# Performance work log

Hardware: AMD Instinct MI355X
Metric: run time of the kernel (lower is better)

Reference implementation:

```python
import jax, jax.numpy as jnp
import numpy as np

L = 12      # n_layers
C = 768     # n_embd = dim = dim_att
H = 12      # heads
N = 64      # head_size_a
FF = 2688   # dim_ffn = int(768*3.5//32*32)
P = 2       # patch_size
INCH = 4
IMG = 32
NCLS = 1000
FREQ = 256
HC = C // 2  # conv stem channels (dim//2)
B = 32
D_MIX = 32
D_DEC = 64
LNX_EPS = 1e-5 * 8.0 ** 2  # GroupNorm eps with head_size_divisor=8


def _ln(x, w=None, b=None, eps=1e-5):
    m = x.mean(-1, keepdims=True)
    v = x.var(-1, keepdims=True)
    xh = (x - m) * jax.lax.rsqrt(v + eps)
    if w is not None:
        xh = xh * w + b
    return xh


def _shift(x):  # RWKV token shift: prepend zero row, drop last
    return jnp.pad(x, ((0, 0), (1, 0), (0, 0)))[:, :-1]


def _gn_img(x, w, b, groups=32, eps=1e-5):
    Bb, Ch, Hh, Ww = x.shape
    xg = x.reshape(Bb, groups, Ch // groups, Hh, Ww)
    m = xg.mean((2, 3, 4), keepdims=True)
    v = xg.var((2, 3, 4), keepdims=True)
    xg = (xg - m) * jax.lax.rsqrt(v + eps)
    return xg.reshape(Bb, Ch, Hh, Ww) * w[None, :, None, None] + b[None, :, None, None]


def _conv5(x, w, b):
    y = jax.lax.conv_general_dilated(x, w, (1, 1), ((2, 2), (2, 2)),
                                     dimension_numbers=('NCHW', 'OIHW', 'NCHW'))
    return y + b[None, :, None, None]


def _wkv(r, k, v, w, u):
    # r,k,v,w: (B,T,H,N); u: (H,N). S[b,h,i,j]: key i -> value j.
    def step(S, inp):
        rt, kt, vt, wt = inp  # each (B,H,N)
        kv = kt[..., :, None] * vt[..., None, :]           # (B,H,N,N)
        y = jnp.einsum('bhi,bhij->bhj', rt, S + u[None, :, :, None] * kv)
        S = wt[..., :, None] * S + kv
        return S, y
    S0 = jnp.zeros((r.shape[0], H, N, N), r.dtype)
    seq = tuple(jnp.moveaxis(a, 1, 0) for a in (r, k, v, w))
    _, ys = jax.lax.scan(step, S0, seq)
    return jnp.moveaxis(ys, 0, 1)  # (B,T,H,N)


def _timemix(x, p):
    Bb, Tt, _ = x.shape
    xx = _shift(x) - x
    xxx = x + xx * p['maa'][0]
    mix = jnp.tanh(xxx @ p['tm_w1']).reshape(Bb, Tt, 5, D_MIX)
    m = jnp.einsum('btfd,fdc->fbtc', mix, p['tm_w2'])  # (5,B,T,C): mw,mk,mv,mr,mg
    xw = x + xx * (p['maa'][1] + m[0])
    xk = x + xx * (p['maa'][2] + m[1])
    xv = x + xx * (p['maa'][3] + m[2])
    xr = x + xx * (p['maa'][4] + m[3])
    xg = x + xx * (p['maa'][5] + m[4])
    r = (xr @ p['r_w'].T).reshape(Bb, Tt, H, N)
    k = (xk @ p['k_w'].T).reshape(Bb, Tt, H, N)
    v = (xv @ p['v_w'].T).reshape(Bb, Tt, H, N)
    g = jax.nn.silu(xg @ p['g_w'].T)
    ww = p['td'] + jnp.tanh(xw @ p['td_w1']) @ p['td_w2']
    w = jnp.exp(-jnp.exp(ww)).reshape(Bb, Tt, H, N)
    y = _wkv(r, k, v, w, p['faaaa'])  # (B,T,H,N)
    mn = y.mean(-1, keepdims=True)
    vr = y.var(-1, keepdims=True)
    y = ((y - mn) * jax.lax.rsqrt(vr + LNX_EPS)).reshape(Bb, Tt, C) * p['lnx_w'] + p['lnx_b']
    return (y * g) @ p['o_w'].T


def _chanmix(x, p):
    xx = _shift(x) - x
    xk = x + xx * p['fmaa'][0]
    xr = x + xx * p['fmaa'][1]
    k = jnp.square(jax.nn.relu(xk @ p['fk_w'].T))
    return jax.nn.sigmoid(xr @ p['fr_w'].T) * (k @ p['fv_w'].T)


def _forward(x, t, y, c1_w, c1_b, gn1_w, gn1_b, c2_w, c2_b, gn2_w, gn2_b,
             xe_w, xe_b, te_w1, te_b1, te_w2, te_b2, y_tab, ln0_w, ln0_b,
             ln1_w, ln1_b, ln2_w, ln2_b, att_maa, tm_w1, tm_w2, td, td_w1,
             td_w2, faaaa, r_w, k_w, v_w, o_w, g_w, lnx_w, lnx_b, ffn_maa,
             fk_w, fr_w, fv_w, ada_w, ada_b, fl_ada_w, fl_ada_b, fl_w, fl_b):
    Bb = x.shape[0]
    h = jax.nn.silu(_conv5(x, c1_w, c1_b))
    h = _gn_img(h, gn1_w, gn1_b)
    h = jax.nn.silu(_conv5(h, c2_w, c2_b))
    h = _gn_img(h, gn2_w, gn2_b)
    # patchify: (B,HC,IMG,IMG) -> (B,T,P*P*HC)
    G = IMG // P
    h = h.reshape(Bb, HC, G, P, G, P).transpose(0, 2, 4, 1, 3, 5).reshape(Bb, G * G, HC * P * P)
    xs = h @ xe_w.T + xe_b
    # timestep embedding
    half = FREQ // 2
    freqs = jnp.exp(-jnp.log(10000.0) * jnp.arange(half, dtype=jnp.float32) / half)
    ang = t[:, None] * freqs[None]
    temb = jnp.concatenate([jnp.cos(ang), jnp.sin(ang)], -1)
    temb = jax.nn.silu(temb @ te_w1.T + te_b1) @ te_w2.T + te_b2
    c = temb + y_tab[y]  # adaln_input (B,C)
    for l in range(L):
        ada = jax.nn.silu(c) @ ada_w[l].T + ada_b[l]
        sm, scm, gm, sp, scp, gp = jnp.split(ada, 6, axis=1)
        if l == 0:
            xs = _ln(xs, ln0_w, ln0_b)
        p = dict(maa=att_maa[l], tm_w1=tm_w1[l], tm_w2=tm_w2[l], td=td[l],
                 td_w1=td_w1[l], td_w2=td_w2[l], faaaa=faaaa[l], r_w=r_w[l],
                 k_w=k_w[l], v_w=v_w[l], o_w=o_w[l], g_w=g_w[l], lnx_w=lnx_w[l],
                 lnx_b=lnx_b[l], fmaa=ffn_maa[l], fk_w=fk_w[l], fr_w=fr_w[l],
                 fv_w=fv_w[l])
        hmod = _ln(xs, ln1_w[l], ln1_b[l]) * (1 + scm[:, None, :]) + sm[:, None, :]
        xs = xs + gm[:, None, :] * _timemix(hmod, p)
        hmod = _ln(xs, ln2_w[l], ln2_b[l]) * (1 + scp[:, None, :]) + sp[:, None, :]
        xs = xs + gp[:, None, :] * _chanmix(hmod, p)
    ada = jax.nn.silu(c) @ fl_ada_w.T + fl_ada_b
    sh, sc = jnp.split(ada, 2, axis=1)
    out = (_ln(xs, eps=1e-6) * (1 + sc[:, None, :]) + sh[:, None, :]) @ fl_w.T + fl_b
    G = IMG // P
    out = out.reshape(Bb, G, G, P, P, INCH)
    out = jnp.einsum('nhwpqc->nchpwq', out).reshape(Bb, INCH, IMG, IMG)
    return out


def setup_inputs() -> dict:
    key = jax.random.key(0)
    ks = iter(jax.random.split(key, 64))
    def rn(shape, s=0.02):
        return (jax.random.normal(next(ks), shape) * s).astype(jnp.float32)
    inp = {}
    inp['x'] = jax.random.normal(next(ks), (B, INCH, IMG, IMG), jnp.float32)
    inp['t'] = jax.random.uniform(next(ks), (B,), jnp.float32) * 1000.0
    inp['y'] = jax.random.randint(next(ks), (B,), 0, NCLS)
    inp['c1_w'] = rn((HC, INCH, 5, 5), 0.05); inp['c1_b'] = jnp.zeros(HC)
    inp['gn1_w'] = jnp.ones(HC); inp['gn1_b'] = jnp.zeros(HC)
    inp['c2_w'] = rn((HC, HC, 5, 5), 0.02); inp['c2_b'] = jnp.zeros(HC)
    inp['gn2_w'] = jnp.ones(HC); inp['gn2_b'] = jnp.zeros(HC)
    inp['xe_w'] = rn((C, P * P * HC)); inp['xe_b'] = jnp.zeros(C)
    inp['te_w1'] = rn((C, FREQ)); inp['te_b1'] = jnp.zeros(C)
    inp['te_w2'] = rn((C, C)); inp['te_b2'] = jnp.zeros(C)
    inp['y_tab'] = rn((NCLS + 1, C))
    inp['ln0_w'] = jnp.ones(C); inp['ln0_b'] = jnp.zeros(C)
    inp['ln1_w'] = jnp.ones((L, C)); inp['ln1_b'] = jnp.zeros((L, C))
    inp['ln2_w'] = jnp.ones((L, C)); inp['ln2_b'] = jnp.zeros((L, C))
    inp['att_maa'] = jax.random.uniform(next(ks), (L, 6, C), jnp.float32)
    inp['tm_w1'] = rn((L, C, 5 * D_MIX), 0.01)
    inp['tm_w2'] = rn((L, 5, D_MIX, C), 0.01)
    inp['td'] = rn((L, C), 0.5) - 3.0
    inp['td_w1'] = rn((L, C, D_DEC), 0.01)
    inp['td_w2'] = rn((L, D_DEC, C), 0.01)
    inp['faaaa'] = rn((L, H, N), 0.1)
    for nm in ('r_w', 'k_w', 'v_w', 'o_w', 'g_w'):
        inp[nm] = rn((L, C, C))
    inp['lnx_w'] = jnp.ones((L, C)); inp['lnx_b'] = jnp.zeros((L, C))
    inp['ffn_maa'] = jax.random.uniform(next(ks), (L, 2, C), jnp.float32)
    inp['fk_w'] = rn((L, FF, C)); inp['fr_w'] = rn((L, C, C)); inp['fv_w'] = rn((L, C, FF))
    inp['ada_w'] = rn((L, 6 * C, C)); inp['ada_b'] = jnp.zeros((L, 6 * C))
    inp['fl_ada_w'] = rn((2 * C, C)); inp['fl_ada_b'] = jnp.zeros(2 * C)
    inp['fl_w'] = rn((P * P * INCH, C)); inp['fl_b'] = jnp.zeros(P * P * INCH)
    return inp


def reference(x, t, y, c1_w, c1_b, gn1_w, gn1_b, c2_w, c2_b, gn2_w, gn2_b,
              xe_w, xe_b, te_w1, te_b1, te_w2, te_b2, y_tab, ln0_w, ln0_b,
              ln1_w, ln1_b, ln2_w, ln2_b, att_maa, tm_w1, tm_w2, td, td_w1,
              td_w2, faaaa, r_w, k_w, v_w, o_w, g_w, lnx_w, lnx_b, ffn_maa,
              fk_w, fr_w, fv_w, ada_w, ada_b, fl_ada_w, fl_ada_b, fl_w, fl_b):
    return _forward(x, t, y, c1_w, c1_b, gn1_w, gn1_b, c2_w, c2_b, gn2_w, gn2_b,
                    xe_w, xe_b, te_w1, te_b1, te_w2, te_b2, y_tab, ln0_w, ln0_b,
                    ln1_w, ln1_b, ln2_w, ln2_b, att_maa, tm_w1, tm_w2, td, td_w1,
                    td_w2, faaaa, r_w, k_w, v_w, o_w, g_w, lnx_w, lnx_b, ffn_maa,
                    fk_w, fr_w, fv_w, ada_w, ada_b, fl_ada_w, fl_ada_b, fl_w, fl_b)
```

## Files before the change

kernel.cpp:

```cpp
#include <hip/hip_runtime.h>
#include <math.h>


typedef short  s16x8 __attribute__((ext_vector_type(8)));
typedef float  f32x4 __attribute__((ext_vector_type(4)));
typedef __attribute__((address_space(1))) const void as1_cv;
typedef __attribute__((address_space(3))) void as3_v;

#define GLDS16(gp, lp) __builtin_amdgcn_global_load_lds( \
    (as1_cv*)(unsigned long long)(const void*)(gp), \
    (as3_v*)(unsigned int)(unsigned long long)(void*)(lp), 16, 0, 0)

static __device__ __forceinline__ float sigf(float x){ return 1.f/(1.f+expf(-x)); }
static __device__ __forceinline__ unsigned short f2b(float x){
  unsigned int u = __builtin_bit_cast(unsigned int, x);
  unsigned int r = (u + 0x7FFFu + ((u >> 16) & 1u)) >> 16;
  return (unsigned short)r;
}
static __device__ __forceinline__ float b2f(unsigned short h){
  unsigned int u = ((unsigned int)h)<<16; return __builtin_bit_cast(float,u);
}

static const size_t O_XS    = 0ull;
static const size_t O_HMOD  = 6291456ull;
// ... 199 lines not shown
  const int wr = w >> 1, wc = w & 1;
  const int l15 = lane & 15, l4 = lane >> 4;
  const int kkc = ((lane & 7) ^ (lane >> 3)) * 8;
  const int N = gr.N;
  f32x4 acc[4][4] = {};
  for (int k0 = 0; k0 < K; k0 += 64) {
    #pragma unroll
    for (int i = 0; i < 4; i++) {
      const int rb = i*32 + w*8;
      const int r  = rb + (lane >> 3);
      GLDS16(gr.A + (size_t)(row0 + r)*K + k0 + kkc, &As[rb][0]);
      GLDS16(gr.B + (size_t)(col0 + r)*K + k0 + kkc, &Bs[rb][0]);
    }
    __syncthreads();
    #pragma unroll
    for (int ks = 0; ks < 2; ks++) {
      s16x8 af[4], bf[4];
      #pragma unroll
      for (int m = 0; m < 4; m++) {
        const int r = wr*64 + m*16 + l15;
        const int sl = (ks*4 + l4) ^ (r & 7);
        af[m] = *reinterpret_cast<const s16x8*>(&As[r][sl*8]);
      }
      #pragma unroll
      for (int n = 0; n < 4; n++) {
        const int r = wc*64 + n*16 + l15;
        const int sl = (ks*4 + l4) ^ (r & 7);
        bf[n] = *reinterpret_cast<const s16x8*>(&Bs[r][sl*8]);
      }
      #pragma unroll
      for (int m = 0; m < 4; m++)
        #pragma unroll
        for (int n = 0; n < 4; n++)
          acc[m][n] = __builtin_amdgcn_mfma_f32_16x16x32_bf16(af[m], bf[n], acc[m][n], 0, 0, 0);
    }
    __syncthreads();
  }
  float* Cf = (float*)gr.C; unsigned short* Ch = (unsigned short*)gr.C;
  #pragma unroll
  for (int m = 0; m < 4; m++) {
    const int rbase = row0 + wr*64 + m*16 + (l4<<2);
    #pragma unroll
    for (int n = 0; n < 4; n++) {
      const int c = col0 + wc*64 + n*16 + l15;
      #pragma unroll
      for (int q = 0; q < 4; q++) {
        const int r = rbase + q;
        float v = acc[m][n][q];
        const size_t idx = (size_t)r*N + c;
        switch (gr.epi) {
          case 0: Cf[idx] = v; break;
          case 1: Cf[idx] = v*sigf(v); break;
          case 2: Cf[idx] = sigf(v); break;
          default: { float t=fmaxf(v,0.f); Ch[idx] = f2b(t*t); } break;
        }
      }
    }
  }
}

__global__ __launch_bounds__(256) void conv1_k(
    const float* __restrict__ x, const float* __restrict__ w,
    const float* __restrict__ bias, float* __restrict__ out)
{
  const int blk = blockIdx.x; const int bb = blk / 384; const int oc = blk % 384;
  __shared__ __align__(16) float sIn[4*1296];
  __shared__ __align__(16) float sW[100];
  const int tid = threadIdx.x;
  for (int idx=tid; idx<4*1296; idx+=256){
    int ic = idx/1296; int rem = idx - ic*1296;
    int yy = rem/36, xx = rem - yy*36;
    int gy = yy-2, gx = xx-2;
    float v = 0.f;
    if ((unsigned)gy < 32u && (unsigned)gx < 32u)
      v = x[(((size_t)bb*4+ic)*32+gy)*32+gx];
    sIn[idx]=v;
  }
  if (tid < 100) sW[tid] = w[(size_t)oc*100 + tid];
  __syncthreads();
  const float bv = bias[oc];
  #pragma unroll
  for (int i=0;i<4;i++){
    int p = tid + 256*i; int py=p>>5, px=p&31;
    int pb = py*36+px;
    float acc = bv;
    #pragma unroll
    for (int ic=0;ic<4;ic++)
      #pragma unroll
      for (int ky=0;ky<5;ky++)
        #pragma unroll
        for (int kx=0;kx<5;kx++)
          acc = fmaf(sIn[ic*1296 + pb + ky*36+kx], sW[ic*25+ky*5+kx], acc);
    out[((size_t)(bb*384+oc))*1024 + p] = acc*sigf(acc);
  }
}

__global__ __launch_bounds__(256) void gn_stats_nchw_k(
    const float* __restrict__ h, float* __restrict__ stats)
{
  const int blk = blockIdx.x;
  const size_t base = (size_t)blk*12288;
  const int tid = threadIdx.x;
  float s=0.f, s2=0.f;
  for (int idx=tid; idx<12288; idx+=256){ float v=h[base+idx]; s+=v; s2=fmaf(v,v,s2); }
  #pragma unroll
  for (int mask=32; mask>=1; mask>>=1){ s += __shfl_xor(s,mask); s2 += __shfl_xor(s2,mask); }
  __shared__ float ps[8];
// ... 1 lines not shown
  __syncthreads();
  if (tid==0){
    s = ps[0]+ps[1]+ps[2]+ps[3]; s2 = ps[4]+ps[5]+ps[6]+ps[7];
    float mean = s*(1.f/12288.f);
    float var  = s2*(1.f/12288.f) - mean*mean;
    stats[blk*2] = mean; stats[blk*2+1] = rsqrtf(var + 1e-5f);
  }
}

__global__ void zero16_k(unsigned short* __restrict__ p)
{
  size_t i = ((size_t)blockIdx.x*256 + threadIdx.x)*8;
  *reinterpret_cast<uint4*>(p + i) = make_uint4(0u,0u,0u,0u);
}

__global__ __launch_bounds__(256) void pad_apply_k(
    const float* __restrict__ img1, const float* __restrict__ stats,
    const float* __restrict__ w, const float* __restrict__ bgn,
    unsigned short* __restrict__ pad)
{
  __shared__ float t[8][33];
  const int b = blockIdx.x >> 5, y = blockIdx.x & 31;
  const int tid = threadIdx.x;
  for (int ic0 = 0; ic0 < 384; ic0 += 8) {
    const int icr = tid >> 5, xr = tid & 31;
    t[icr][xr] = img1[(((size_t)b*384 + ic0+icr)*32 + y)*32 + xr];
    __syncthreads();
    const int xw_ = tid >> 3, icw = tid & 7;
    const int ch = ic0 + icw;
    const int g = ch / 12;
    const float mean = stats[(b*32+g)*2], rstd = stats[(b*32+g)*2+1];
    float v = (t[icw][xw_] - mean)*rstd*w[ch] + bgn[ch];
    pad[(((size_t)b*36 + y+2)*36 + (xw_+2))*384 + ch] = f2b(v);
    __syncthreads();
  }
}

__global__ __launch_bounds__(256) void wrepack_k(
    const float* __restrict__ w, unsigned short* __restrict__ wtap)
{
  __shared__ float t[9600];
  const int oc = blockIdx.x; const int tid = threadIdx.x;
  for (int i=tid;i<9600;i+=256) t[i] = w[(size_t)oc*9600 + i];
  __syncthreads();
  for (int i=tid;i<9600;i+=256){
    int tap=i/384, ic=i-tap*384;
    wtap[((size_t)tap*384 + oc)*384 + ic] = f2b(t[ic*25+tap]);
  }
}

__global__ __launch_bounds__(256) void conv2m_k(
    const unsigned short* __restrict__ inp,
    const unsigned short* __restrict__ wtap,
    const float* __restrict__ bias, float* __restrict__ out)
{
  __shared__ __align__(16) unsigned short As[128][64];
  __shared__ __align__(16) unsigned short Bs[128][64];
  const int blk = blockIdx.x;
  const int b = blk / 24, rem = blk % 24, pt = rem / 3, ot = rem % 3;
  const int y0 = pt * 4, oc0 = ot * 128;
  const int tid = threadIdx.x, w = tid>>6, lane = tid&63;
  const int wr = w>>1, wc = w&1;
  const int l15 = lane & 15, l4 = lane >> 4;
  const int kkc = ((lane&7) ^ (lane>>3)) * 8;
  f32x4 acc[4][4] = {};
  for (int dy = 0; dy < 5; dy++) {
    for (int dx = 0; dx < 5; dx++) {
      const int tap = dy*5 + dx;
      for (int ic0 = 0; ic0 < 384; ic0 += 64) {
        #pragma unroll
        for (int i = 0; i < 4; i++) {
          const int rb = i*32 + w*8;
          const int r = rb + (lane>>3);
          const int py = r >> 5, px = r & 31;
          GLDS16(inp + (((size_t)(b*36 + y0+py+dy))*36 + (px+dx))*384 + ic0 + kkc, &As[rb][0]);
          GLDS16(wtap + ((size_t)tap*384 + oc0 + r)*384 + ic0 + kkc, &Bs[rb][0]);
        }
        __syncthreads();
        #pragma unroll
        for (int ks = 0; ks < 2; ks++) {
          s16x8 af[4], bf[4];
          #pragma unroll
          for (int m = 0; m < 4; m++) {
            const int r = wr*64 + m*16 + l15;
            const int sl = (ks*4 + l4) ^ (r & 7);
            af[m] = *reinterpret_cast<const s16x8*>(&As[r][sl*8]);
          }
          #pragma unroll
          for (int n = 0; n < 4; n++) {
            const int r = wc*64 + n*16 + l15;
            const int sl = (ks*4 + l4) ^ (r & 7);
            bf[n] = *reinterpret_cast<const s16x8*>(&Bs[r][sl*8]);
          }
          #pragma unroll
          for (int m = 0; m < 4; m++)
            #pragma unroll
            for (int n = 0; n < 4; n++)
              acc[m][n] = __builtin_amdgcn_mfma_f32_16x16x32_bf16(af[m], bf[n], acc[m][n], 0, 0, 0);
        }
        __syncthreads();
      }
    }
  }
  #pragma unroll
  for (int m = 0; m < 4; m++) {
    #pragma unroll
    for (int n = 0; n < 4; n++) {
      const int oc = oc0 + wc*64 + n*16 + l15;
      const float bv = bias[oc];
      #pragma unroll
      for (int q = 0; q < 4; q++) {
        const int p = wr*64 + m*16 + (l4<<2) + q;
        const int py = p >> 5, px = p & 31;
        float v = acc[m][n][q] + bv;
        out[((size_t)b*1024 + (y0+py)*32 + px)*384 + oc] = v*sigf(v);
      }
    }
  }
}

__global__ __launch_bounds__(256) void gn_stats_nhwc_k(
    const float* __restrict__ h, float* __restrict__ stats)
{
  const int b = blockIdx.x >> 5, g = blockIdx.x & 31;
  const int tid = threadIdx.x;
  float s=0.f, s2=0.f;
  for (int idx=tid; idx<12288; idx+=256){
    int p = idx/12, c = idx - p*12;
    float v = h[((size_t)b*1024+p)*384 + g*12 + c];
    s+=v; s2=fmaf(v,v,s2);
  }
  #pragma unroll
  for (int mask=32; mask>=1; mask>>=1){ s += __shfl_xor(s,mask); s2 += __shfl_xor(s2,mask); }
  __shared__ float ps[8];
  if ((tid&63)==0){ ps[tid>>6]=s; ps[4+(tid>>6)]=s2; }
  __syncthreads();
  if (tid==0){
    s = ps[0]+ps[1]+ps[2]+ps[3]; s2 = ps[4]+ps[5]+ps[6]+ps[7];
    float mean = s*(1.f/12288.f);
    float var  = s2*(1.f/12288.f) - mean*mean;
    stats[(b*32+g)*2] = mean; stats[(b*32+g)*2+1] = rsqrtf(var + 1e-5f);
  }
}

__global__ void patchify_gn_k(const float* __restrict__ h, const float* __restrict__ stats,
                              const float* __restrict__ w, const float* __restrict__ bgn,
                              unsigned short* __restrict__ pm)
{
  int idx = blockIdx.x*256 + threadIdx.x;
  int row = idx/1536, f = idx - row*1536;
  int c = f>>2; int p=(f>>1)&1; int q=f&1;
  int bb=row>>8; int tok=row&255; int gh=tok>>4, gw=tok&15;
  int pix = (gh*2+p)*32 + gw*2+q;
  int g = c / 12;
  float mean = stats[(bb*32+g)*2], rstd = stats[(bb*32+g)*2+1];
  float v = (h[((size_t)bb*1024 + pix)*384 + c] - mean)*rstd*w[c] + bgn[c];
  pm[idx] = f2b(v);
}

__global__ void temb_in_k(const float* __restrict__ t, float* __restrict__ out)
{
  int bb = blockIdx.x; int i = threadIdx.x;
  float fr = expf(-logf(10000.f) * (float)i / 128.f);
  float ang = t[bb]*fr;
  out[bb*256+i]     = cosf(ang);
  out[bb*256+128+i] = sinf(ang);
}

__global__ void siluc_k(const float* __restrict__ t2, const float* __restrict__ ytab,
                        const int* __restrict__ y, float* __restrict__ sc)
{
  int bb = blockIdx.x; int tid = threadIdx.x;
  int cls = y[bb];
  for (int c=tid; c<768; c+=256){
    float v = t2[bb*768+c] + ytab[(size_t)cls*768+c];
    sc[bb*768+c] = v*sigf(v);
  }
}

__global__ __launch_bounds__(256) void ln_mod_k(
    const float* __restrict__ in, float* __restrict__ out,
    const float* __restrict__ w, const float* __restrict__ b,
    const float* __restrict__ mod, int mstride, int sh_off, int sc_off, float eps)
{
  const int m = blockIdx.x; const int tid = threadIdx.x;
  const size_t base = (size_t)m*768;
  float v0=in[base+tid], v1=in[base+tid+256], v2=in[base+tid+512];
  float s = v0+v1+v2;
  float s2 = fmaf(v0,v0,fmaf(v1,v1,v2*v2));
  #pragma unroll
  for (int mask=32; mask>=1; mask>>=1){ s += __shfl_xor(s,mask); s2 += __shfl_xor(s2,mask); }
  __shared__ float ps[8];
  if ((tid&63)==0){ ps[tid>>6]=s; ps[4+(tid>>6)]=s2; }
  __syncthreads();
  s = ps[0]+ps[1]+ps[2]+ps[3]; s2 = ps[4]+ps[5]+ps[6]+ps[7];
  const float mean = s*(1.f/768.f);
  const float var  = s2*(1.f/768.f) - mean*mean;
  const float rstd = rsqrtf(var + eps);
  const int bb = m >> 8;
  #pragma unroll
  for (int k=0;k<3;k++){
    const int c = tid + k*256;
    float v = (k==0)?v0:((k==1)?v1:v2);
    float xh = (v-mean)*rstd;
    if (w) xh = fmaf(xh, w[c], b[c]);
    if (mod){
      float scv = mod[(size_t)bb*mstride + sc_off + c];
      float shv = mod[(size_t)bb*mstride + sh_off + c];
      xh = fmaf(xh, 1.f+scv, shv);
// ... 97 lines not shown
    const unsigned short* __restrict__ mix16, const float* __restrict__ w2,
    const float* __restrict__ hmod, const float* __restrict__ xx,
    const float* __restrict__ maa15,
    unsigned short* __restrict__ xw, unsigned short* __restrict__ xk,
    unsigned short* __restrict__ xv, unsigned short* __restrict__ xr,
    unsigned short* __restrict__ xg)
{
  __shared__ __align__(16) float smix[16][160];
  const int m0 = blockIdx.x * 16;
  const int tid = threadIdx.x;
  for (int idx=tid; idx<16*160; idx+=256){
    int r = idx/160, d = idx - r*160;
    smix[r][d] = b2f(mix16[(size_t)(m0+r)*160 + d]);
  }
  __syncthreads();
  #pragma unroll 1
  for (int cc=0; cc<3; cc++){
    const int c = tid + cc*256;
    float hv[16], xv_[16];
    #pragma unroll
    for (int r=0;r<16;r++){ size_t id=(size_t)(m0+r)*768+c; hv[r]=hmod[id]; xv_[r]=xx[id]; }
    #pragma unroll 1
    for (int f=0; f<5; f++){
      float acc[16];
      const float base = maa15[f*768 + c];
      #pragma unroll
      for (int r=0;r<16;r++) acc[r]=base;
      #pragma unroll 1
      for (int d4=0; d4<8; d4++){
        float wv[4];
        #pragma unroll
        for (int q=0;q<4;q++) wv[q] = w2[(size_t)(f*32+d4*4+q)*768 + c];
        #pragma unroll
        for (int r=0;r<16;r++){
          const float4 mv = *reinterpret_cast<const float4*>(&smix[r][f*32+d4*4]);
          acc[r] = fmaf(mv.x,wv[0],fmaf(mv.y,wv[1],fmaf(mv.z,wv[2],fmaf(mv.w,wv[3],acc[r]))));
        }
      }
      #pragma unroll
      for (int r=0;r<16;r++){
        float val = fmaf(xv_[r], acc[r], hv[r]);
        size_t id = (size_t)(m0+r)*768+c;
        if (f==0) xw[id]=f2b(val);
        else if (f==1) xk[id]=f2b(val);
        else if (f==2) xv[id]=f2b(val);
        else if (f==3) xr[id]=f2b(val);
        else           xg[id]=f2b(val);
      }
    }
  }
}

__global__ __launch_bounds__(256) void wkv_k(
    const float* __restrict__ r, const float* __restrict__ k,
    const float* __restrict__ v, const float* __restrict__ wde,
    const float* __restrict__ g, const float* __restrict__ u,
    const float* __restrict__ lnxw, const float* __restrict__ lnxb,
    unsigned short* __restrict__ out16)
{
  const int bh = blockIdx.x; const int b = bh/12, h = bh%12;
  const int tid = threadIdx.x;
  const int q = tid >> 6, j = tid & 63;
  __shared__ __align__(16) float sbuf[5][32][64];
  __shared__ float yred[2][4][64];
  const size_t gbase = (size_t)(b*256)*768 + h*64;

  float S[16];
  #pragma unroll
  for (int i=0;i<16;i++) S[i]=0.f;
  float u16[16];
  #pragma unroll
  for (int i=0;i<16;i++) u16[i] = u[h*64 + q*16 + i];
  const float lw_r = lnxw[h*64+j], lb_r = lnxb[h*64+j];

  float4 pf[10];
  #define WKV_LOAD(c_) { \
    const size_t cb = gbase + (size_t)(c_)*32*768; \
    _Pragma("unroll") \
    for (int p=0;p<10;p++){ \
      const int a = p>>1; \
      const int ii = ((p&1)<<10) + tid*4; \
      const float* sp = (a==0)?r:(a==1)?k:(a==2)?wde:(a==3)?v:g; \
      pf[p] = *reinterpret_cast<const float4*>(sp + cb + (size_t)(ii>>6)*768 + (ii&63)); \
    } }

  WKV_LOAD(0);
  #pragma unroll 1
  for (int c=0; c<8; c++){
    __syncthreads();
    #pragma unroll
    for (int p=0;p<10;p++){
      const int a = p>>1;
      const int ii = ((p&1)<<10) + tid*4;
      *reinterpret_cast<float4*>(&sbuf[a][ii>>6][ii&63]) = pf[p];
    }
    __syncthreads();
    if (c<7) WKV_LOAD(c+1);
    #pragma unroll 1
    for (int tt=0; tt<32; tt++){
      const int t = c*32+tt;
      const float vj = sbuf[3][tt][j];
      float yp = 0.f;
      #pragma unroll
      for (int ii=0; ii<16; ii+=4){
        const float4 r4 = *reinterpret_cast<const float4*>(&sbuf[0][tt][q*16+ii]);
        const float4 k4 = *reinterpret_cast<const float4*>(&sbuf[1][tt][q*16+ii]);
        const float4 w4 = *reinterpret_cast<const float4*>(&sbuf[2][tt][q*16+ii]);
        float kv;
        kv=k4.x*vj; yp += r4.x*fmaf(u16[ii+0],kv,S[ii+0]); S[ii+0]=fmaf(w4.x,S[ii+0],kv);
        kv=k4.y*vj; yp += r4.y*fmaf(u16[ii+1],kv,S[ii+1]); S[ii+1]=fmaf(w4.y,S[ii+1],kv);
        kv=k4.z*vj; yp += r4.z*fmaf(u16[ii+2],kv,S[ii+2]); S[ii+2]=fmaf(w4.z,S[ii+2],kv);
        kv=k4.w*vj; yp += r4.w*fmaf(u16[ii+3],kv,S[ii+3]); S[ii+3]=fmaf(w4.w,S[ii+3],kv);
      }
      yred[t&1][q][j] = yp;
      __syncthreads();
      if (q == (t&3)) {
        const float yo = yred[t&1][0][j]+yred[t&1][1][j]+yred[t&1][2][j]+yred[t&1][3][j];
        float s = yo, s2 = yo*yo;
        #pragma unroll
        for (int mask=32; mask>=1; mask>>=1){ s += __shfl_xor(s,mask); s2 += __shfl_xor(s2,mask); }
        const float mean = s*(1.f/64.f);
        const float var  = s2*(1.f/64.f) - mean*mean;
        const float xh = (yo-mean)*rsqrtf(var + 6.4e-4f);
        out16[gbase + (size_t)t*768 + j] = f2b(fmaf(xh, lw_r, lb_r) * sbuf[4][tt][j]);
      }
    }
  }
  #undef WKV_LOAD
}

__global__ void unpatch_k(const float* __restrict__ po, float* __restrict__ out)
{
  int idx = blockIdx.x*256 + threadIdx.x;
  int xq=idx&31; int yy=(idx>>5)&31; int ch=(idx>>10)&3; int bb=idx>>12;
  int gh=yy>>1, p=yy&1, gw=xq>>1, q=xq&1;
  out[idx] = po[((size_t)(bb*256+gh*16+gw))*16 + p*8+q*4+ch];
}

__global__ void f2b_k(const float* __restrict__ s, unsigned short* __restrict__ d)
{
  size_t i = ((size_t)blockIdx.x*256 + threadIdx.x)*8;
  float4 a = *reinterpret_cast<const float4*>(s+i);
  float4 b = *reinterpret_cast<const float4*>(s+i+4);
  s16x8 o;
  o[0]=(short)f2b(a.x); o[1]=(short)f2b(a.y); o[2]=(short)f2b(a.z); o[3]=(short)f2b(a.w);
  o[4]=(short)f2b(b.x); o[5]=(short)f2b(b.y); o[6]=(short)f2b(b.z); o[7]=(short)f2b(b.w);
  *reinterpret_cast<s16x8*>(d + i) = o;
}

__global__ void f2b_layer_k(
    const float* __restrict__ r_, const float* __restrict__ k_, const float* __restrict__ v_,
    const float* __restrict__ o_, const float* __restrict__ g_, const float* __restrict__ fr_,
    const float* __restrict__ fk_, const float* __restrict__ fv_,
    unsigned short* __restrict__ dst)
{
  size_t i = ((size_t)blockIdx.x*256 + threadIdx.x)*8;
  const float* s; size_t off;
  if (i < 3538944) {
    unsigned seg = (unsigned)(i / 589824u); off = i - (size_t)seg*589824u;
    s = seg==0?r_:seg==1?k_:seg==2?v_:seg==3?o_:seg==4?g_:fr_;
  } else if (i < 5603328) { s = fk_; off = i - 3538944; }
  else                    { s = fv_; off = i - 5603328; }
  float4 a = *reinterpret_cast<const float4*>(s+off);
  float4 b = *reinterpret_cast<const float4*>(s+off+4);
  s16x8 o;
  o[0]=(short)f2b(a.x); o[1]=(short)f2b(a.y); o[2]=(short)f2b(a.z); o[3]=(short)f2b(a.w);
  o[4]=(short)f2b(b.x); o[5]=(short)f2b(b.y); o[6]=(short)f2b(b.z); o[7]=(short)f2b(b.w);
  *reinterpret_cast<s16x8*>(dst + i) = o;
}

__global__ void wmix_repack_k(const float* __restrict__ tm1, const float* __restrict__ td1,
                              const float* __restrict__ td2, unsigned short* __restrict__ dst)
{
  int idx = blockIdx.x*256 + threadIdx.x;
  if (idx < 196608) {
    int n = idx/768, k = idx - n*768;
    dst[idx] = (n<160) ? f2b(tm1[(size_t)k*160 + n]) : (unsigned short)0;
  } else if (idx < 294912) {
    int i = idx-196608; int n = i/768, k = i - n*768;
    dst[idx] = (n<64) ? f2b(td1[(size_t)k*64 + n]) : (unsigned short)0;
  } else {
// ... 14 lines not shown
  const float* gn1w  = (const float*)d_in[5];
  const float* gn1b  = (const float*)d_in[6];
  const float* c2w   = (const float*)d_in[7];
  const float* c2b   = (const float*)d_in[8];
  const float* gn2w  = (const float*)d_in[9];
  const float* gn2b  = (const float*)d_in[10];
  const float* xew   = (const float*)d_in[11];
  const float* xeb   = (const float*)d_in[12];
  const float* tew1  = (const float*)d_in[13];
  const float* teb1  = (const float*)d_in[14];
  const float* tew2  = (const float*)d_in[15];
  const float* teb2  = (const float*)d_in[16];
  const float* ytab  = (const float*)d_in[17];
  const float* ln0w  = (const float*)d_in[18];
  const float* ln0b  = (const float*)d_in[19];
  const float* ln1w  = (const float*)d_in[20];
  const float* ln1b  = (const float*)d_in[21];
  const float* ln2w  = (const float*)d_in[22];
  const float* ln2b  = (const float*)d_in[23];
  const float* amaa  = (const float*)d_in[24];
  const float* tmw1  = (const float*)d_in[25];
  const float* tmw2  = (const float*)d_in[26];
  const float* tdv   = (const float*)d_in[27];
  const float* tdw1  = (const float*)d_in[28];
  const float* tdw2  = (const float*)d_in[29];
  const float* faa   = (const float*)d_in[30];
  const float* rw    = (const float*)d_in[31];
  const float* kw    = (const float*)d_in[32];
  const float* vw    = (const float*)d_in[33];
  const float* ow    = (const float*)d_in[34];
  const float* gw    = (const float*)d_in[35];
  const float* lnxw  = (const float*)d_in[36];
  const float* lnxb  = (const float*)d_in[37];
  const float* fmaa  = (const float*)d_in[38];
  const float* fkw   = (const float*)d_in[39];
  const float* frw   = (const float*)d_in[40];
  const float* fvw   = (const float*)d_in[41];
  const float* adaw  = (const float*)d_in[42];
  const float* adab  = (const float*)d_in[43];
  const float* flaw  = (const float*)d_in[44];
  const float* flab  = (const float*)d_in[45];
  const float* flw   = (const float*)d_in[46];
  const float* flb   = (const float*)d_in[47];

  float* Wf = (float*)d_ws;
  float* xs   = Wf+O_XS;   float* hmod = Wf+O_HMOD;
  float* ada  = Wf+O_ADA;  float* fla  = Wf+O_FLA;
  float* t2   = Wf+O_T2;   float* sc   = Wf+O_SC;
  float* ti   = Wf+O_TI;   float* t1   = Wf+O_T1;
  float* st1  = Wf+O_ST1;  float* st2  = Wf+O_ST2;
  unsigned short* xew16 = (unsigned short*)(Wf+O_XEW16);
  unsigned short* wl16  = (unsigned short*)(Wf+O_WL16);
  float* big = Wf+O_BIG;
  float* xxb  = big+L_XX;  float* rb = big+L_XXX;
  float* kb   = big+L_KB;  float* vb   = big+L_VB;  float* gb = big+L_GB;
  float* wd   = big+L_WD;
  unsigned short* xw16  = (unsigned short*)(big+L_XW);
  unsigned short* xxx16 = (unsigned short*)(big+L_XXX);
  unsigned short* mixb16= (unsigned short*)(big+L_MIXB);
  unsigned short* wt16  = (unsigned short*)(big+L_WT);
  unsigned short* xk16 = (unsigned short*)(big+L_XK16);
  unsigned short* xv16 = (unsigned short*)(big+L_XV16);
  unsigned short* xr16 = (unsigned short*)(big+L_XR16);
  unsigned short* xg16 = (unsigned short*)(big+L_XG16);
  unsigned short* gnh16 = (unsigned short*)(big+L_GNH16);
  unsigned short* kbig16 = (unsigned short*)(big+L_KBIG16);
  float* img1 = big+S_IMG1; float* img2 = big+S_IMG2;
  unsigned short* pad16  = (unsigned short*)(big+S_PAD16);
  unsigned short* wtap16 = (unsigned short*)(big+S_WTAP16);
  unsigned short* pm16   = (unsigned short*)(big+S_PM16);
  float* pout = big+L_MIXB;
  unsigned short* dr  = wl16;
  unsigned short* dk  = wl16 + 589824;
  unsigned short* dv  = wl16 + 1179648;
  unsigned short* do_ = wl16 + 1769472;
  unsigned short* dg  = wl16 + 2359296;
  unsigned short* dfr = wl16 + 2949120;
  unsigned short* dfk = wl16 + 3538944;
  unsigned short* dfv = wl16 + 5603328;
  unsigned short* dtm1t = wl16 + 7667712;
  unsigned short* dtd1t = wl16 + 7864320;
  unsigned short* dtd2t = wl16 + 7962624;

  conv1_k<<<dim3(32*384),dim3(256),0,stream>>>(x_in, c1w, c1b, img1);
  gn_stats_nchw_k<<<dim3(1024),dim3(256),0,stream>>>(img1, st1);
  zero16_k<<<dim3(7776),dim3(256),0,stream>>>(pad16);
  pad_apply_k<<<dim3(1024),dim3(256),0,stream>>>(img1, st1, gn1w, gn1b, pad16);
  wrepack_k<<<dim3(384),dim3(256),0,stream>>>(c2w, wtap16);
  conv2m_k<<<dim3(768),dim3(256),0,stream>>>(pad16, wtap16, c2b, img2);
  gn_stats_nhwc_k<<<dim3(1024),dim3(256),0,stream>>>(img2, st2);
  patchify_gn_k<<<dim3(49152),dim3(256),0,stream>>>(img2, st2, gn2w, gn2b, pm16);
  f2b_k<<<dim3(576),dim3(256),0,stream>>>(xew, xew16);
  BGEMM(BEPI_BIAS_F32, pm16, xew16, xs, xeb, nullptr,nullptr,0, 8192,768,1536);

  temb_in_k<<<dim3(32),dim3(128),0,stream>>>(t_in, ti);
  GEMM(EPI_SILU,true, ti, tew1, t1, teb1, 32,768,256);
  GEMM(EPI_NONE,true, t1, tew2, t2, teb2, 32,768,768);
  siluc_k<<<dim3(32),dim3(256),0,stream>>>(t2, ytab, y_in, sc);
  GEMM(EPI_NONE,true, sc, adaw, ada, adab, 32,55296,768);
  GEMM(EPI_NONE,true, sc, flaw, fla, flab, 32,1536,768);

  ln_mod_k<<<dim3(8192),dim3(256),0,stream>>>(xs, xs, ln0w, ln0b, nullptr, 0,0,0, 1e-5f);

  for (int l=0; l<12; l++){
    const float* adal = ada + (size_t)l*4608;
    f2b_layer_k<<<dim3(3744),dim3(256),0,stream>>>(
        rw+(size_t)l*589824, kw+(size_t)l*589824, vw+(size_t)l*589824,
        ow+(size_t)l*589824, gw+(size_t)l*589824, frw+(size_t)l*589824,
        fkw+(size_t)l*2064384, fvw+(size_t)l*2064384, wl16);
    wmix_repack_k<<<dim3(1344),dim3(256),0,stream>>>(
        tmw1+(size_t)l*122880, tdw1+(size_t)l*49152, tdw2+(size_t)l*49152, dtm1t);
    ln_shift_tm_k<<<dim3(8192),dim3(256),0,stream>>>(
        xs, ln1w+(size_t)l*768, ln1b+(size_t)l*768, adal, amaa+(size_t)l*4608,
        hmod, xxb, xxx16);
    BGEMM(BEPI_TANH_BF16, xxx16, dtm1t, mixb16, nullptr,nullptr,nullptr,0, 8192,160,768);
    five_mix_k<<<dim3(512),dim3(256),0,stream>>>(mixb16, tmw2+(size_t)l*122880, hmod, xxb,
                                                 amaa+(size_t)l*4608+768, xw16,xk16,xv16,xr16,xg16);
    BGEMM(BEPI_TANH_BF16, xw16, dtd1t, wt16, nullptr,nullptr,nullptr,0, 8192,64,768);
    BGEMM(BEPI_WDEC_F32, wt16, dtd2t, wd, nullptr, tdv+(size_t)l*768, nullptr,0, 8192,768,64);
    {
      BGrp4 G;
      G.g[0].A=xr16; G.g[0].B=dr; G.g[0].C=rb; G.g[0].epi=0; G.g[0].N=768; G.g[0].gx=6;
      G.g[1].A=xk16; G.g[1].B=dk; G.g[1].C=kb; G.g[1].epi=0; G.g[1].N=768; G.g[1].gx=6;
      G.g[2].A=xv16; G.g[2].B=dv; G.g[2].C=vb; G.g[2].epi=0; G.g[2].N=768; G.g[2].gx=6;
      G.g[3].A=xg16; G.g[3].B=dg; G.g[3].C=gb; G.g[3].epi=1; G.g[3].N=768; G.g[3].gx=6;
      bgemm_grp_k<<<dim3(6,64,4),dim3(256),0,stream>>>(G, 8192, 768);
    }
    wkv_k<<<dim3(384),dim3(256),0,stream>>>(rb, kb, vb, wd, gb, faa+(size_t)l*768,
                                            lnxw+(size_t)l*768, lnxb+(size_t)l*768, gnh16);
    BGEMM(BEPI_RES_GM, gnh16, do_, xs, nullptr, adal+1536, nullptr, 55296, 8192,768,768);
    ln_shift_cm_k<<<dim3(8192),dim3(256),0,stream>>>(
        xs, ln2w+(size_t)l*768, ln2b+(size_t)l*768, adal, fmaa+(size_t)l*1536, xk16, xr16);
    {
      BGrp4 G;
      G.g[0].A=xk16; G.g[0].B=dfk; G.g[0].C=kbig16; G.g[0].epi=3; G.g[0].N=2688; G.g[0].gx=21;
      G.g[1].A=xr16; G.g[1].B=dfr; G.g[1].C=gb;     G.g[1].epi=2; G.g[1].N=768;  G.g[1].gx=6;
      G.g[2]=G.g[1]; G.g[3]=G.g[1];
      bgemm_grp_k<<<dim3(21,64,2),dim3(256),0,stream>>>(G, 8192, 768);
    }
    BGEMM(BEPI_RES_GP, kbig16, dfv, xs, nullptr, adal+3840, gb, 55296, 8192,768,2688);
  }

  ln_mod_k<<<dim3(8192),dim3(256),0,stream>>>(xs, hmod, nullptr, nullptr, fla, 1536, 0, 768, 1e-6f);
  GEMM(EPI_NONE,true, hmod, flw, pout, flb, 8192,16,768);
  unpatch_k<<<dim3(512),dim3(256),0,stream>>>(pout, (float*)d_out);
}
```

Measured before the change: 10.28 ms.

## Rewrite WKV as chunked MFMA form and store r/k/v/g and conv2 output in bf16

The per-timestep serial WKV recurrence is replaced by a chunked formulation. Within each 32-step chunk, cumulative decay products rescale r and k, the intra-chunk attention matrix and the cross-chunk state contribution are computed with bf16 MFMA, and the state is updated once per chunk. The r/k/v/g projection GEMMs now write bf16 instead of fp32, and conv2's output feeding the group norm is also stored in bf16; conv2's loop order is changed to put channels outermost. This cuts memory traffic and the long serial dependency chain, at the cost of bf16 precision in the state and a division by cumulative decay products that can grow large or underflow.

```diff
diff --git a/kernel.cpp b/kernel.cpp
--- a/kernel.cpp
+++ b/kernel.cpp
@@ -275,7 +275,9 @@
           case 0: Cf[idx] = v; break;
           case 1: Cf[idx] = v*sigf(v); break;
           case 2: Cf[idx] = sigf(v); break;
-          default: { float t=fmaxf(v,0.f); Ch[idx] = f2b(t*t); } break;
+          case 3: { float t=fmaxf(v,0.f); Ch[idx] = f2b(t*t); } break;
+          case 4: Ch[idx] = f2b(v); break;
+          default: Ch[idx] = f2b(v*sigf(v)); break;
         }
       }
     }
@@ -383,7 +385,7 @@
 __global__ __launch_bounds__(256) void conv2m_k(
     const unsigned short* __restrict__ inp,
     const unsigned short* __restrict__ wtap,
-    const float* __restrict__ bias, float* __restrict__ out)
+    const float* __restrict__ bias, unsigned short* __restrict__ out)
 {
   __shared__ __align__(16) unsigned short As[128][64];
   __shared__ __align__(16) unsigned short Bs[128][64];
@@ -395,10 +397,10 @@
   const int l15 = lane & 15, l4 = lane >> 4;
   const int kkc = ((lane&7) ^ (lane>>3)) * 8;
   f32x4 acc[4][4] = {};
-  for (int dy = 0; dy < 5; dy++) {
-    for (int dx = 0; dx < 5; dx++) {
-      const int tap = dy*5 + dx;
-      for (int ic0 = 0; ic0 < 384; ic0 += 64) {
+  for (int ic0 = 0; ic0 < 384; ic0 += 64) {
+    for (int dy = 0; dy < 5; dy++) {
+      for (int dx = 0; dx < 5; dx++) {
+        const int tap = dy*5 + dx;
         #pragma unroll
         for (int i = 0; i < 4; i++) {
           const int rb = i*32 + w*8;
@@ -444,21 +446,21 @@
         const int p = wr*64 + m*16 + (l4<<2) + q;
         const int py = p >> 5, px = p & 31;
         float v = acc[m][n][q] + bv;
-        out[((size_t)b*1024 + (y0+py)*32 + px)*384 + oc] = v*sigf(v);
+        out[((size_t)b*1024 + (y0+py)*32 + px)*384 + oc] = f2b(v*sigf(v));
       }
     }
   }
 }
 
 __global__ __launch_bounds__(256) void gn_stats_nhwc_k(
-    const float* __restrict__ h, float* __restrict__ stats)
+    const unsigned short* __restrict__ h, float* __restrict__ stats)
 {
   const int b = blockIdx.x >> 5, g = blockIdx.x & 31;
   const int tid = threadIdx.x;
   float s=0.f, s2=0.f;
   for (int idx=tid; idx<12288; idx+=256){
     int p = idx/12, c = idx - p*12;
-    float v = h[((size_t)b*1024+p)*384 + g*12 + c];
+    float v = b2f(h[((size_t)b*1024+p)*384 + g*12 + c]);
     s+=v; s2=fmaf(v,v,s2);
   }
   #pragma unroll
@@ -474,7 +476,7 @@
   }
 }
 
-__global__ void patchify_gn_k(const float* __restrict__ h, const float* __restrict__ stats,
+__global__ void patchify_gn_k(const unsigned short* __restrict__ h, const float* __restrict__ stats,
                               const float* __restrict__ w, const float* __restrict__ bgn,
                               unsigned short* __restrict__ pm)
 {
@@ -485,7 +487,7 @@
   int pix = (gh*2+p)*32 + gw*2+q;
   int g = c / 12;
   float mean = stats[(bb*32+g)*2], rstd = stats[(bb*32+g)*2+1];
-  float v = (h[((size_t)bb*1024 + pix)*384 + c] - mean)*rstd*w[c] + bgn[c];
+  float v = (b2f(h[((size_t)bb*1024 + pix)*384 + c]) - mean)*rstd*w[c] + bgn[c];
   pm[idx] = f2b(v);
 }
 
@@ -689,81 +691,204 @@
 }
 
 __global__ __launch_bounds__(256) void wkv_k(
-    const float* __restrict__ r, const float* __restrict__ k,
-    const float* __restrict__ v, const float* __restrict__ wde,
-    const float* __restrict__ g, const float* __restrict__ u,
+    const unsigned short* __restrict__ rg, const unsigned short* __restrict__ kg,
+    const unsigned short* __restrict__ vg, const float* __restrict__ wg,
+    const unsigned short* __restrict__ gg, const float* __restrict__ u,
     const float* __restrict__ lnxw, const float* __restrict__ lnxb,
     unsigned short* __restrict__ out16)
 {
   const int bh = blockIdx.x; const int b = bh/12, h = bh%12;
   const int tid = threadIdx.x;
-  const int q = tid >> 6, j = tid & 63;
-  __shared__ __align__(16) float sbuf[5][32][64];
-  __shared__ float yred[2][4][64];
-  const size_t gbase = (size_t)(b*256)*768 + h*64;
-
-  float S[16];
-  #pragma unroll
-  for (int i=0;i<16;i++) S[i]=0.f;
-  float u16[16];
-  #pragma unroll
-  for (int i=0;i<16;i++) u16[i] = u[h*64 + q*16 + i];
-  const float lw_r = lnxw[h*64+j], lb_r = lnxb[h*64+j];
-
-  float4 pf[10];
-  #define WKV_LOAD(c_) { \
-    const size_t cb = gbase + (size_t)(c_)*32*768; \
-    _Pragma("unroll") \
-    for (int p=0;p<10;p++){ \
-      const int a = p>>1; \
-      const int ii = ((p&1)<<10) + tid*4; \
-      const float* sp = (a==0)?r:(a==1)?k:(a==2)?wde:(a==3)?v:g; \
-      pf[p] = *reinterpret_cast<const float4*>(sp + cb + (size_t)(ii>>6)*768 + (ii&63)); \
-    } }
-
-  WKV_LOAD(0);
+  const int w = tid >> 6, lane = tid & 63;
+  const int l4 = lane >> 4, l15 = lane & 15;
+  __shared__ __align__(16) unsigned short r16s[32][64], k16s[32][64], v16s[32][64], g16s[32][64];
+  __shared__ __align__(16) float wds[32][64];
+  __shared__ __align__(16) float Wl[33][64];
+  __shared__ __align__(16) unsigned short rr16[32][64], kk16[32][64];
+  __shared__ __align__(16) unsigned short kk2T[64][32], vT[64][32];
+  __shared__ __align__(16) unsigned short S16T[64][64];
+  __shared__ __align__(16) unsigned short A16[32][32];
+  __shared__ float diag[32], ypsum[32][4], ypsq[32][4];
+
+  reinterpret_cast<uint4*>(&S16T[0][0])[tid] = make_uint4(0,0,0,0);
+  reinterpret_cast<uint4*>(&S16T[0][0])[256+tid] = make_uint4(0,0,0,0);
+
+  const float u_lane = u[h*64 + lane];
+  const int jj = w*16 + l15;
+  const float lw = lnxw[h*64 + jj], lb = lnxb[h*64 + jj];
+  const size_t gb = (size_t)(b*256)*768 + h*64;
+
+  const int st_t = tid >> 3, st_i = (tid & 7) * 8;
+  uint4 pr, pk, pv, pg; float4 pw0, pw1;
+
+#define WKV_LOADC(c_) { \
+    const size_t tb = gb + (size_t)((c_)*32 + st_t)*768 + st_i; \
+    pr = *reinterpret_cast<const uint4*>(rg + tb); \
+    pk = *reinterpret_cast<const uint4*>(kg + tb); \
+    pv = *reinterpret_cast<const uint4*>(vg + tb); \
+    pg = *reinterpret_cast<const uint4*>(gg + tb); \
+    pw0 = *reinterpret_cast<const float4*>(wg + tb); \
+    pw1 = *reinterpret_cast<const float4*>(wg + tb + 4); }
+#define WKV_STAGE() { \
+    *reinterpret_cast<uint4*>(&r16s[st_t][st_i]) = pr; \
+    *reinterpret_cast<uint4*>(&k16s[st_t][st_i]) = pk; \
+    *reinterpret_cast<uint4*>(&v16s[st_t][st_i]) = pv; \
+    *reinterpret_cast<uint4*>(&g16s[st_t][st_i]) = pg; \
+    *reinterpret_cast<float4*>(&wds[st_t][st_i]) = pw0; \
+    *reinterpret_cast<float4*>(&wds[st_t][st_i+4]) = pw1; }
+
+  f32x4 S_acc[4] = {};
+
+  WKV_LOADC(0);
+  WKV_STAGE();
+  __syncthreads();
+
   #pragma unroll 1
-  for (int c=0; c<8; c++){
+  for (int c = 0; c < 8; ++c) {
+    if (w == 0) {
+      float wv[32];
+      #pragma unroll
+      for (int t=0;t<32;t++) wv[t] = wds[t][lane];
+      float P = 1.f;
+      Wl[0][lane] = 1.f;
+      #pragma unroll
+      for (int t=0;t<32;t++){ P *= wv[t]; Wl[t+1][lane] = P; }
+    }
     __syncthreads();
-    #pragma unroll
-    for (int p=0;p<10;p++){
-      const int a = p>>1;
-      const int ii = ((p&1)<<10) + tid*4;
-      *reinterpret_cast<float4*>(&sbuf[a][ii>>6][ii&63]) = pf[p];
+    {
+      const int t = st_t, i0 = st_i;
+      s16x8 rv = *reinterpret_cast<const s16x8*>(&r16s[t][i0]);
+      s16x8 kv = *reinterpret_cast<const s16x8*>(&k16s[t][i0]);
+      s16x8 vv = *reinterpret_cast<const s16x8*>(&v16s[t][i0]);
+      float4 wa0 = *reinterpret_cast<const float4*>(&Wl[t][i0]);
+      float4 wa1 = *reinterpret_cast<const float4*>(&Wl[t][i0+4]);
+      float4 wb0 = *reinterpret_cast<const float4*>(&Wl[t+1][i0]);
+      float4 wb1 = *reinterpret_cast<const float4*>(&Wl[t+1][i0+4]);
+      float4 wf0 = *reinterpret_cast<const float4*>(&Wl[32][i0]);
+      float4 wf1 = *reinterpret_cast<const float4*>(&Wl[32][i0+4]);
+      float wt_[8] = {wa0.x,wa0.y,wa0.z,wa0.w,wa1.x,wa1.y,wa1.z,wa1.w};
+      float wt1[8] = {wb0.x,wb0.y,wb0.z,wb0.w,wb1.x,wb1.y,wb1.z,wb1.w};
+      float w32[8] = {wf0.x,wf0.y,wf0.z,wf0.w,wf1.x,wf1.y,wf1.z,wf1.w};
+      s16x8 rro, kko;
+      #pragma unroll
+      for (int e=0;e<8;e++){
+        const int i = i0 + e;
+        float rf = b2f((unsigned short)rv[e]) * wt_[e];
+        float kf = b2f((unsigned short)kv[e]) / wt1[e];
+        rro[e] = (short)f2b(rf);
+        kko[e] = (short)f2b(kf);
+        kk2T[i][(((t>>3)^(i&3))<<3) + (t&7)] = f2b(kf * w32[e]);
+        vT[i][(((t>>3)^(i&3))<<3) + (t&7)] = (unsigned short)vv[e];
+      }
+      const int sc_ = ((i0>>3)^(t&7))<<3;
+      *reinterpret_cast<s16x8*>(&rr16[t][sc_]) = rro;
+      *reinterpret_cast<s16x8*>(&kk16[t][sc_]) = kko;
+      #pragma unroll
+      for (int tt=0;tt<8;tt++){
+        const int td = w*8 + tt;
+        float p = b2f(r16s[td][lane]) * u_lane * b2f(k16s[td][lane]);
+        #pragma unroll
+        for (int mask=32; mask>=1; mask>>=1) p += __shfl_xor(p, mask);
+        if (lane==0) diag[td] = p;
+      }
     }
     __syncthreads();
-    if (c<7) WKV_LOAD(c+1);
-    #pragma unroll 1
-    for (int tt=0; tt<32; tt++){
-      const int t = c*32+tt;
-      const float vj = sbuf[3][tt][j];
-      float yp = 0.f;
-      #pragma unroll
-      for (int ii=0; ii<16; ii+=4){
-        const float4 r4 = *reinterpret_cast<const float4*>(&sbuf[0][tt][q*16+ii]);
-        const float4 k4 = *reinterpret_cast<const float4*>(&sbuf[1][tt][q*16+ii]);
-        const float4 w4 = *reinterpret_cast<const float4*>(&sbuf[2][tt][q*16+ii]);
-        float kv;
-        kv=k4.x*vj; yp += r4.x*fmaf(u16[ii+0],kv,S[ii+0]); S[ii+0]=fmaf(w4.x,S[ii+0],kv);
-        kv=k4.y*vj; yp += r4.y*fmaf(u16[ii+1],kv,S[ii+1]); S[ii+1]=fmaf(w4.y,S[ii+1],kv);
-        kv=k4.z*vj; yp += r4.z*fmaf(u16[ii+2],kv,S[ii+2]); S[ii+2]=fmaf(w4.z,S[ii+2],kv);
-        kv=k4.w*vj; yp += r4.w*fmaf(u16[ii+3],kv,S[ii+3]); S[ii+3]=fmaf(w4.w,S[ii+3],kv);
-      }
-      yred[t&1][q][j] = yp;
+    if (c < 7) WKV_LOADC(c+1);
+    f32x4 Y[2] = {};
+    s16x8 rrf[2][2];
+    #pragma unroll
+    for (int m=0;m<2;m++)
+      #pragma unroll
+      for (int kt=0;kt<2;kt++){
+        const int row = m*16 + l15;
+        rrf[m][kt] = *reinterpret_cast<const s16x8*>(&rr16[row][(((kt*4+l4)^(row&7))<<3)]);
+      }
+    #pragma unroll
+    for (int m=0;m<2;m++)
+      #pragma unroll
+      for (int kt=0;kt<2;kt++){
+        s16x8 sf = *reinterpret_cast<const s16x8*>(&S16T[jj][(((kt*4+l4)^(jj&7))<<3)]);
+        Y[m] = __builtin_amdgcn_mfma_f32_16x16x32_bf16(rrf[m][kt], sf, Y[m], 0,0,0);
+      }
+    s16x8 vtf = *reinterpret_cast<const s16x8*>(&vT[jj][((l4^(jj&3))<<3)]);
+    #pragma unroll
+    for (int m=0;m<4;m++){
+      const int row = m*16 + l15;
+      s16x8 k2f = *reinterpret_cast<const s16x8*>(&kk2T[row][((l4^(row&3))<<3)]);
+      #pragma unroll
+      for (int q=0;q<4;q++) S_acc[m][q] *= Wl[32][m*16 + l4*4 + q];
+      S_acc[m] = __builtin_amdgcn_mfma_f32_16x16x32_bf16(k2f, vtf, S_acc[m], 0,0,0);
+    }
+    if (w == 0) {
+      f32x4 Aac[2][2] = {};
+      #pragma unroll
+      for (int m=0;m<2;m++)
+        #pragma unroll
+        for (int n=0;n<2;n++)
+          #pragma unroll
+          for (int kt=0;kt<2;kt++){
+            const int srow = n*16 + l15;
+            s16x8 kf = *reinterpret_cast<const s16x8*>(&kk16[srow][(((kt*4+l4)^(srow&7))<<3)]);
+            Aac[m][n] = __builtin_amdgcn_mfma_f32_16x16x32_bf16(rrf[m][kt], kf, Aac[m][n], 0,0,0);
+          }
+      #pragma unroll
+      for (int m=0;m<2;m++)
+        #pragma unroll
+        for (int n=0;n<2;n++)
+          #pragma unroll
+          for (int q=0;q<4;q++){
+            const int t = m*16 + l4*4 + q;
+            const int s = n*16 + l15;
+            float av = Aac[m][n][q];
+            av = (s < t) ? av : ((s == t) ? diag[t] : 0.f);
+            A16[t][(((s>>3)^(t&3))<<3) + (s&7)] = f2b(av);
+          }
+    }
+    #pragma unroll
+    for (int m=0;m<4;m++)
+      #pragma unroll
+      for (int q=0;q<4;q++){
+        const int i = m*16 + l4*4 + q;
+        S16T[jj][(((i>>3)^(jj&7))<<3) + (i&7)] = f2b(S_acc[m][q]);
+      }
+    __syncthreads();
+    #pragma unroll
+    for (int m=0;m<2;m++){
+      const int row = m*16 + l15;
+      s16x8 af = *reinterpret_cast<const s16x8*>(&A16[row][((l4^(row&3))<<3)]);
+      Y[m] = __builtin_amdgcn_mfma_f32_16x16x32_bf16(af, vtf, Y[m], 0,0,0);
+    }
+    #pragma unroll
+    for (int m=0;m<2;m++)
+      #pragma unroll
+      for (int q=0;q<4;q++){
+        float s1 = Y[m][q], s2 = s1*s1;
+        #pragma unroll
+        for (int mask=8; mask>=1; mask>>=1){ s1 += __shfl_xor(s1,mask); s2 += __shfl_xor(s2,mask); }
+        if (l15==0){ const int t = m*16 + l4*4 + q; ypsum[t][w]=s1; ypsq[t][w]=s2; }
+      }
+    __syncthreads();
+    #pragma unroll
+    for (int m=0;m<2;m++)
+      #pragma unroll
+      for (int q=0;q<4;q++){
+        const int t = m*16 + l4*4 + q;
+        float s1 = ypsum[t][0]+ypsum[t][1]+ypsum[t][2]+ypsum[t][3];
+        float s2 = ypsq[t][0]+ypsq[t][1]+ypsq[t][2]+ypsq[t][3];
+        float mean = s1*(1.f/64.f);
+        float var  = s2*(1.f/64.f) - mean*mean;
+        float xh = (Y[m][q]-mean)*rsqrtf(var + 6.4e-4f);
+        float o = fmaf(xh, lw, lb) * b2f(g16s[t][jj]);
+        out16[gb + (size_t)(c*32+t)*768 + jj] = f2b(o);
+      }
+    if (c < 7) {
       __syncthreads();
-      if (q == (t&3)) {
-        const float yo = yred[t&1][0][j]+yred[t&1][1][j]+yred[t&1][2][j]+yred[t&1][3][j];
-        float s = yo, s2 = yo*yo;
-        #pragma unroll
-        for (int mask=32; mask>=1; mask>>=1){ s += __shfl_xor(s,mask); s2 += __shfl_xor(s2,mask); }
-        const float mean = s*(1.f/64.f);
-        const float var  = s2*(1.f/64.f) - mean*mean;
-        const float xh = (yo-mean)*rsqrtf(var + 6.4e-4f);
-        out16[gbase + (size_t)t*768 + j] = f2b(fmaf(xh, lw_r, lb_r) * sbuf[4][tt][j]);
-      }
-    }
-  }
-  #undef WKV_LOAD
+      WKV_STAGE();
+      __syncthreads();
+    }
+  }
+#undef WKV_LOADC
+#undef WKV_STAGE
 }
 
 __global__ void unpatch_k(const float* __restrict__ po, float* __restrict__ out)
@@ -884,9 +1009,13 @@
   unsigned short* xew16 = (unsigned short*)(Wf+O_XEW16);
   unsigned short* wl16  = (unsigned short*)(Wf+O_WL16);
   float* big = Wf+O_BIG;
-  float* xxb  = big+L_XX;  float* rb = big+L_XXX;
-  float* kb   = big+L_KB;  float* vb   = big+L_VB;  float* gb = big+L_GB;
+  float* xxb  = big+L_XX;
   float* wd   = big+L_WD;
+  float* gbf  = big+L_GB;
+  unsigned short* rb16  = (unsigned short*)(big+L_XXX);
+  unsigned short* kb16  = (unsigned short*)(big+L_KB);
+  unsigned short* vb16  = (unsigned short*)(big+L_VB);
+  unsigned short* gb16  = (unsigned short*)(big+L_GB);
   unsigned short* xw16  = (unsigned short*)(big+L_XW);
   unsigned short* xxx16 = (unsigned short*)(big+L_XXX);
   unsigned short* mixb16= (unsigned short*)(big+L_MIXB);
@@ -897,7 +1026,8 @@
   unsigned short* xg16 = (unsigned short*)(big+L_XG16);
   unsigned short* gnh16 = (unsigned short*)(big+L_GNH16);
   unsigned short* kbig16 = (unsigned short*)(big+L_KBIG16);
-  float* img1 = big+S_IMG1; float* img2 = big+S_IMG2;
+  float* img1 = big+S_IMG1;
+  unsigned short* img2_16 = (unsigned short*)(big+S_IMG2);
   unsigned short* pad16  = (unsigned short*)(big+S_PAD16);
   unsigned short* wtap16 = (unsigned short*)(big+S_WTAP16);
   unsigned short* pm16   = (unsigned short*)(big+S_PM16);
@@ -919,9 +1049,9 @@
   zero16_k<<<dim3(7776),dim3(256),0,stream>>>(pad16);
   pad_apply_k<<<dim3(1024),dim3(256),0,stream>>>(img1, st1, gn1w, gn1b, pad16);
   wrepack_k<<<dim3(384),dim3(256),0,stream>>>(c2w, wtap16);
-  conv2m_k<<<dim3(768),dim3(256),0,stream>>>(pad16, wtap16, c2b, img2);
-  gn_stats_nhwc_k<<<dim3(1024),dim3(256),0,stream>>>(img2, st2);
-  patchify_gn_k<<<dim3(49152),dim3(256),0,stream>>>(img2, st2, gn2w, gn2b, pm16);
+  conv2m_k<<<dim3(768),dim3(256),0,stream>>>(pad16, wtap16, c2b, img2_16);
+  gn_stats_nhwc_k<<<dim3(1024),dim3(256),0,stream>>>(img2_16, st2);
+  patchify_gn_k<<<dim3(49152),dim3(256),0,stream>>>(img2_16, st2, gn2w, gn2b, pm16);
   f2b_k<<<dim3(576),dim3(256),0,stream>>>(xew, xew16);
   BGEMM(BEPI_BIAS_F32, pm16, xew16, xs, xeb, nullptr,nullptr,0, 8192,768,1536);
 
@@ -952,13 +1082,13 @@
     BGEMM(BEPI_WDEC_F32, wt16, dtd2t, wd, nullptr, tdv+(size_t)l*768, nullptr,0, 8192,768,64);
     {
       BGrp4 G;
-      G.g[0].A=xr16; G.g[0].B=dr; G.g[0].C=rb; G.g[0].epi=0; G.g[0].N=768; G.g[0].gx=6;
-      G.g[1].A=xk16; G.g[1].B=dk; G.g[1].C=kb; G.g[1].epi=0; G.g[1].N=768; G.g[1].gx=6;
-      G.g[2].A=xv16; G.g[2].B=dv; G.g[2].C=vb; G.g[2].epi=0; G.g[2].N=768; G.g[2].gx=6;
-      G.g[3].A=xg16; G.g[3].B=dg; G.g[3].C=gb; G.g[3].epi=1; G.g[3].N=768; G.g[3].gx=6;
+      G.g[0].A=xr16; G.g[0].B=dr; G.g[0].C=rb16; G.g[0].epi=4; G.g[0].N=768; G.g[0].gx=6;
+      G.g[1].A=xk16; G.g[1].B=dk; G.g[1].C=kb16; G.g[1].epi=4; G.g[1].N=768; G.g[1].gx=6;
+      G.g[2].A=xv16; G.g[2].B=dv; G.g[2].C=vb16; G.g[2].epi=4; G.g[2].N=768; G.g[2].gx=6;
+      G.g[3].A=xg16; G.g[3].B=dg; G.g[3].C=gb16; G.g[3].epi=5; G.g[3].N=768; G.g[3].gx=6;
       bgemm_grp_k<<<dim3(6,64,4),dim3(256),0,stream>>>(G, 8192, 768);
     }
-    wkv_k<<<dim3(384),dim3(256),0,stream>>>(rb, kb, vb, wd, gb, faa+(size_t)l*768,
+    wkv_k<<<dim3(384),dim3(256),0,stream>>>(rb16, kb16, vb16, wd, gb16, faa+(size_t)l*768,
                                             lnxw+(size_t)l*768, lnxb+(size_t)l*768, gnh16);
     BGEMM(BEPI_RES_GM, gnh16, do_, xs, nullptr, adal+1536, nullptr, 55296, 8192,768,768);
     ln_shift_cm_k<<<dim3(8192),dim3(256),0,stream>>>(
@@ -966,11 +1096,11 @@
     {
       BGrp4 G;
       G.g[0].A=xk16; G.g[0].B=dfk; G.g[0].C=kbig16; G.g[0].epi=3; G.g[0].N=2688; G.g[0].gx=21;
-      G.g[1].A=xr16; G.g[1].B=dfr; G.g[1].C=gb;     G.g[1].epi=2; G.g[1].N=768;  G.g[1].gx=6;
+      G.g[1].A=xr16; G.g[1].B=dfr; G.g[1].C=gbf;    G.g[1].epi=2; G.g[1].N=768;  G.g[1].gx=6;
       G.g[2]=G.g[1]; G.g[3]=G.g[1];
       bgemm_grp_k<<<dim3(21,64,2),dim3(256),0,stream>>>(G, 8192, 768);
     }
-    BGEMM(BEPI_RES_GP, kbig16, dfv, xs, nullptr, adal+3840, gb, 55296, 8192,768,2688);
+    BGEMM(BEPI_RES_GP, kbig16, dfv, xs, nullptr, adal+3840, gbf, 55296, 8192,768,2688);
   }
 
   ln_mod_k<<<dim3(8192),dim3(256),0,stream>>>(xs, hmod, nullptr, nullptr, fla, 1536, 0, 768, 1e-6f);
```

Measured after the change: 8.418 ms. 18.1% less time.
